# Kernel optimization log

Measured on AMD Instinct MI355X. Metric: run time of the kernel, lower is better.

Reference implementation:

```python
import jax, jax.numpy as jnp
import numpy as np

N_NODES = 100000
N_EDGES = 3200000
N_GRAPHS = 64
IN_DIM = 64
LATENT = 64
DIST_STD = 1.0


def _gcn_conv(x, W, b, src, dst, dinv):
    """PyG GCNConv: out = D^-1/2 (A+I) D^-1/2 (x W) + b, with dinv = deg^-1/2."""
    n = x.shape[0]
    h = x @ W  # [N, out]
    coef = dinv[src] * dinv[dst]  # per-edge norm
    agg = jax.ops.segment_sum(h[src] * coef[:, None], dst, num_segments=n)
    # self-loop contribution with norm dinv[i]^2
    return agg + h * (dinv * dinv)[:, None] + b


def _mean_pool(x, batch, num_graphs):
    sums = jax.ops.segment_sum(x, batch, num_segments=num_graphs)
    cnts = jax.ops.segment_sum(jnp.ones((x.shape[0],), x.dtype), batch, num_segments=num_graphs)
    return sums / jnp.maximum(cnts, 1.0)[:, None]


def setup_inputs() -> dict:
    key = jax.random.key(0)
    ks = jax.random.split(key, 12)
    x = jax.random.normal(ks[0], (N_NODES, IN_DIM), jnp.float32)
    edge_index = jax.random.randint(ks[1], (2, N_EDGES), 0, N_NODES, jnp.int64 if jax.config.jax_enable_x64 else jnp.int32).astype(jnp.int32)
    batch = jnp.sort(jax.random.randint(ks[2], (N_NODES,), 0, N_GRAPHS)).astype(jnp.int32)

    def glorot(k, shape):
        fan_in, fan_out = shape
        s = jnp.sqrt(6.0 / (fan_in + fan_out))
        return jax.random.uniform(k, shape, jnp.float32, -s, s)

    return {
        "x": x, "edge_index": edge_index, "batch": batch,
        "W1m": glorot(ks[3], (IN_DIM, 16)), "b1m": jnp.zeros((16,), jnp.float32),
        "W2m": glorot(ks[4], (16, 32)), "b2m": jnp.zeros((32,), jnp.float32),
        "W3m": glorot(ks[5], (32, LATENT)), "b3m": jnp.zeros((LATENT,), jnp.float32),
        "W1l": glorot(ks[6], (IN_DIM, 16)), "b1l": jnp.zeros((16,), jnp.float32),
        "W2l": glorot(ks[7], (16, 32)), "b2l": jnp.zeros((32,), jnp.float32),
        "W3l": glorot(ks[8], (32, LATENT)), "b3l": jnp.zeros((LATENT,), jnp.float32),
        "Wfc": glorot(ks[9], (LATENT, 160000)), "bfc": jnp.zeros((160000,), jnp.float32),
        "eps": jax.random.normal(ks[10], (N_GRAPHS, LATENT), jnp.float32) * DIST_STD,
    }


def reference(x, edge_index, batch, W1m, b1m, W2m, b2m, W3m, b3m,
              W1l, b1l, W2l, b2l, W3l, b3l, Wfc, bfc, eps):
    src, dst = edge_index[0], edge_index[1]
    n = x.shape[0]
    # degrees include self-loop (+1)
    deg = jax.ops.segment_sum(jnp.ones((src.shape[0],), x.dtype), dst, num_segments=n) + 1.0
    dinv = jax.lax.rsqrt(deg)

    mu = jax.nn.relu(_gcn_conv(x, W1m, b1m, src, dst, dinv))
    mu = jax.nn.relu(_gcn_conv(mu, W2m, b2m, src, dst, dinv))
    mu = jax.nn.relu(_gcn_conv(mu, W3m, b3m, src, dst, dinv))
    mu = _mean_pool(mu, batch, N_GRAPHS)

    log = jax.nn.relu(_gcn_conv(x, W1l, b1l, src, dst, dinv))
    log = jax.nn.relu(_gcn_conv(log, W2l, b2l, src, dst, dinv))
    log = jax.nn.relu(_gcn_conv(log, W3l, b3l, src, dst, dinv))
    logvar = _mean_pool(log, batch, N_GRAPHS)

    # latent sample (training mode): z = mu + eps * exp(0.5*logvar)
    z = mu + eps * jnp.exp(0.5 * logvar)

    # decode: sigmoid(z Wfc + bfc) -> [G, 400, 400]
    output = jax.nn.sigmoid(z @ Wfc + bfc).reshape(-1, 400, 400)
    return output, mu, logvar
```

## Files before the change

kernel.cpp:

```cpp
#include <hip/hip_runtime.h>
#include <hip/hip_bf16.h>

#define N_NODES 100000
#define N_EDGES 3200000
#define N_GRAPHS 64
#define NB 391
#define KCH 8192
#define NCHUNK ((N_EDGES + KCH - 1) / KCH)
#define MAXBKT 10240
#define NBLK3 (N_NODES / 32)

__device__ __forceinline__ void atomAddF(float* p, float v) {
    unsafeAtomicAdd(p, v);
}

__device__ __forceinline__ float lo2f(unsigned u) { return __uint_as_float(u << 16); }
__device__ __forceinline__ float hi2f(unsigned u) { return __uint_as_float(u & 0xFFFF0000u); }
__device__ __forceinline__ unsigned pack2(float a, float b) {
    unsigned ha = __bfloat16_as_ushort(__float2bfloat16(a));
    unsigned hb = __bfloat16_as_ushort(__float2bfloat16(b));
    return ha | (hb << 16);
}

__global__ __launch_bounds__(512) void k_binCount(const int* __restrict__ dst,
                                                  int* __restrict__ gcount) {
    __shared__ int hist[NB];
    for (int t = threadIdx.x; t < NB; t += 512) hist[t] = 0;
    __syncthreads();
    int base = blockIdx.x * KCH;
    int cnt = min(KCH, N_EDGES - base);
    for (int i = threadIdx.x; i < cnt; i += 512)
        atomicAdd(&hist[dst[base + i] >> 8], 1);
    __syncthreads();
    for (int t = threadIdx.x; t < NB; t += 512)
        if (hist[t]) atomicAdd(&gcount[t], hist[t]);
}

__global__ __launch_bounds__(512) void k_scanB(const int* __restrict__ gcount,
                                               int* __restrict__ gbase,
                                               int* __restrict__ gcursor,
                                               int* __restrict__ rowptr) {
    __shared__ int s[512];
    int v = (threadIdx.x < NB) ? gcount[threadIdx.x] : 0;
    s[threadIdx.x] = v;
    __syncthreads();
    for (int off = 1; off < 512; off <<= 1) {
        int t = (threadIdx.x >= off) ? s[threadIdx.x - off] : 0;
        __syncthreads();
        s[threadIdx.x] += t;
        __syncthreads();
    }
    if (threadIdx.x < NB) {
        int e = s[threadIdx.x] - v;
        gbase[threadIdx.x] = e;
        gcursor[threadIdx.x] = e;
    }
    if (threadIdx.x == 0) rowptr[N_NODES] = N_EDGES;
}

__global__ __launch_bounds__(512) void k_binA(const int* __restrict__ src,
                                              const int* __restrict__ dst,
                                              int* __restrict__ gcursor,
                                              int* __restrict__ binned) {
    __shared__ int hist[512];
    __shared__ int rbase[512];
    hist[threadIdx.x] = 0;
    __syncthreads();
    int base = blockIdx.x * KCH;
    int cnt = min(KCH, N_EDGES - base);
    int pk[16];
    int meta[16];
    #pragma unroll
    for (int i = 0; i < 16; ++i) {
        int idx = i * 512 + threadIdx.x;
        if (idx < cnt) {
            int d = dst[base + idx];
            int b = d >> 8;
            int pos = atomicAdd(&hist[b], 1);
            pk[i] = ((d & 255) << 24) | src[base + idx];
            meta[i] = (b << 13) | pos;
        } else {
            meta[i] = -1;
        }
    }
    __syncthreads();
    if (threadIdx.x < NB) {
        int v = hist[threadIdx.x];
        if (v > 0) rbase[threadIdx.x] = atomicAdd(&gcursor[threadIdx.x], v);
    }
    __syncthreads();
    #pragma unroll
    for (int i = 0; i < 16; ++i) {
        if (meta[i] >= 0) {
            int b = meta[i] >> 13;
            int pos = meta[i] & 8191;
            binned[rbase[b] + pos] = pk[i];
        }
    }
}

__global__ __launch_bounds__(512) void k_passB(const int* __restrict__ gbase,
                                               int* __restrict__ csr,
                                               int* __restrict__ rowptr,
                                               float* __restrict__ dinv) {
    int b = blockIdx.x;
    int rb = gbase[b];
    int re = (b == NB - 1) ? N_EDGES : gbase[b + 1];
    int cnt = re - rb;
    int nbase = b << 8;
    int nn = min(nbase + 256, N_NODES) - nbase;
    __shared__ int stage[MAXBKT];
    __shared__ int nhist[256];
    __shared__ int sc[256];
    __shared__ int ncur[256];
    for (int t = threadIdx.x; t < 256; t += 512) nhist[t] = 0;
    __syncthreads();
    for (int j = threadIdx.x; j < cnt; j += 512) {
        int p = csr[rb + j];
        stage[j] = p;
        atomicAdd(&nhist[((unsigned)p) >> 24], 1);
    }
    __syncthreads();
    if (threadIdx.x < 256) sc[threadIdx.x] = nhist[threadIdx.x];
    __syncthreads();
    for (int off = 1; off < 256; off <<= 1) {
        int t = (threadIdx.x < 256 && threadIdx.x >= off) ? sc[threadIdx.x - off] : 0;
        __syncthreads();
        if (threadIdx.x < 256) sc[threadIdx.x] += t;
        __syncthreads();
    }
    if (threadIdx.x < 256) {
        int e = sc[threadIdx.x] - nhist[threadIdx.x];
        ncur[threadIdx.x] = e;
        if (threadIdx.x < nn) {
            rowptr[nbase + threadIdx.x] = rb + e;
            dinv[nbase + threadIdx.x] = rsqrtf((float)nhist[threadIdx.x] + 1.0f);
        }
    }
    __syncthreads();
    for (int j = threadIdx.x; j < cnt; j += 512) {
        int p = stage[j];
        int slot = atomicAdd(&ncur[((unsigned)p) >> 24], 1);
        csr[rb + slot] = p;
    }
}

template<int LOGW, bool BIAS_RELU, bool OB, bool PRE>
__global__ void __launch_bounds__(256) k_gatherB(
        const int* __restrict__ rowptr, const int* __restrict__ csr,
        const unsigned* __restrict__ in ,
        const float* __restrict__ dinv,
        const float* __restrict__ ba, const float* __restrict__ bb,
        void* __restrict__ out) {
    constexpr int W8 = (1 << LOGW) / 8;
    constexpr int NPB = 256 / W8;
    int n = blockIdx.x * NPB + (threadIdx.x / W8);
    if (n >= N_NODES) return;
    int sub = threadIdx.x % W8;
    const uint4* in4 = (const uint4*)in;
    uint4 u = in4[(size_t)n * W8 + sub];
    float a0 = lo2f(u.x), a1 = hi2f(u.x), a2 = lo2f(u.y), a3 = hi2f(u.y);
    float a4 = lo2f(u.z), a5 = hi2f(u.z), a6 = lo2f(u.w), a7 = hi2f(u.w);
    int j = rowptr[n], end = rowptr[n + 1];
    for (; j + 8 <= end; j += 8) {
        int s0 = csr[j] & 0xFFFFFF;
        int s1 = csr[j + 1] & 0xFFFFFF;
        int s2 = csr[j + 2] & 0xFFFFFF;
        int s3 = csr[j + 3] & 0xFFFFFF;
        int s4 = csr[j + 4] & 0xFFFFFF;
        int s5 = csr[j + 5] & 0xFFFFFF;
        int s6 = csr[j + 6] & 0xFFFFFF;
        int s7 = csr[j + 7] & 0xFFFFFF;
        uint4 v0 = in4[(size_t)s0 * W8 + sub];
        uint4 v1 = in4[(size_t)s1 * W8 + sub];
        uint4 v2 = in4[(size_t)s2 * W8 + sub];
        uint4 v3 = in4[(size_t)s3 * W8 + sub];
        uint4 v4 = in4[(size_t)s4 * W8 + sub];
        uint4 v5 = in4[(size_t)s5 * W8 + sub];
        uint4 v6 = in4[(size_t)s6 * W8 + sub];
        uint4 v7 = in4[(size_t)s7 * W8 + sub];
        a0 += ((lo2f(v0.x) + lo2f(v1.x)) + (lo2f(v2.x) + lo2f(v3.x)))
            + ((lo2f(v4.x) + lo2f(v5.x)) + (lo2f(v6.x) + lo2f(v7.x)));
        a1 += ((hi2f(v0.x) + hi2f(v1.x)) + (hi2f(v2.x) + hi2f(v3.x)))
            + ((hi2f(v4.x) + hi2f(v5.x)) + (hi2f(v6.x) + hi2f(v7.x)));
        a2 += ((lo2f(v0.y) + lo2f(v1.y)) + (lo2f(v2.y) + lo2f(v3.y)))
            + ((lo2f(v4.y) + lo2f(v5.y)) + (lo2f(v6.y) + lo2f(v7.y)));
        a3 += ((hi2f(v0.y) + hi2f(v1.y)) + (hi2f(v2.y) + hi2f(v3.y)))
            + ((hi2f(v4.y) + hi2f(v5.y)) + (hi2f(v6.y) + hi2f(v7.y)));
        a4 += ((lo2f(v0.z) + lo2f(v1.z)) + (lo2f(v2.z) + lo2f(v3.z)))
            + ((lo2f(v4.z) + lo2f(v5.z)) + (lo2f(v6.z) + lo2f(v7.z)));
        a5 += ((hi2f(v0.z) + hi2f(v1.z)) + (hi2f(v2.z) + hi2f(v3.z)))
            + ((hi2f(v4.z) + hi2f(v5.z)) + (hi2f(v6.z) + hi2f(v7.z)));
        a6 += ((lo2f(v0.w) + lo2f(v1.w)) + (lo2f(v2.w) + lo2f(v3.w)))
            + ((lo2f(v4.w) + lo2f(v5.w)) + (lo2f(v6.w) + lo2f(v7.w)));
        a7 += ((hi2f(v0.w) + hi2f(v1.w)) + (hi2f(v2.w) + hi2f(v3.w)))
            + ((hi2f(v4.w) + hi2f(v5.w)) + (hi2f(v6.w) + hi2f(v7.w)));
    }
    for (; j < end; ++j) {
        int s = csr[j] & 0xFFFFFF;
        uint4 v = in4[(size_t)s * W8 + sub];
        a0 += lo2f(v.x); a1 += hi2f(v.x);
        a2 += lo2f(v.y); a3 += hi2f(v.y);
        a4 += lo2f(v.z); a5 += hi2f(v.z);
        a6 += lo2f(v.w); a7 += hi2f(v.w);
    }
    float di = dinv[n];
    a0 *= di; a1 *= di; a2 *= di; a3 *= di;
    a4 *= di; a5 *= di; a6 *= di; a7 *= di;
    if (BIAS_RELU) {
        constexpr int H = (1 << LOGW) / 2;
        int d = sub * 8;
        const float* bp = (d < H) ? (ba + d) : (bb + d - H);
        a0 = fmaxf(a0 + bp[0], 0.0f);
        a1 = fmaxf(a1 + bp[1], 0.0f);
        a2 = fmaxf(a2 + bp[2], 0.0f);
        a3 = fmaxf(a3 + bp[3], 0.0f);
        a4 = fmaxf(a4 + bp[4], 0.0f);
        a5 = fmaxf(a5 + bp[5], 0.0f);
        a6 = fmaxf(a6 + bp[6], 0.0f);
        a7 = fmaxf(a7 + bp[7], 0.0f);
    }
    if (PRE) {
        a0 *= di; a1 *= di; a2 *= di; a3 *= di;
        a4 *= di; a5 *= di; a6 *= di; a7 *= di;
    }
    if (OB) {
        ((uint4*)out)[(size_t)n * W8 + sub] =
            make_uint4(pack2(a0, a1), pack2(a2, a3), pack2(a4, a5), pack2(a6, a7));
    } else {
        constexpr int OUT4 = (1 << LOGW) / 4;
        float4* o4 = (float4*)out;
        o4[(size_t)n * OUT4 + sub * 2]     = make_float4(a0, a1, a2, a3);
        o4[(size_t)n * OUT4 + sub * 2 + 1] = make_float4(a4, a5, a6, a7);
    }
}

#define FMA4(A, W) \
    A.x = fmaf(r, W.x, A.x); A.y = fmaf(r, W.y, A.y); \
    A.z = fmaf(r, W.z, A.z); A.w = fmaf(r, W.w, A.w);

__global__ void __launch_bounds__(256) k_gd2(
        const int* __restrict__ rowptr, const int* __restrict__ csr,
        const unsigned* __restrict__ in,
        const float* __restrict__ dinv,
        const float* __restrict__ W2m, const float* __restrict__ b2m,
        const float* __restrict__ W2l, const float* __restrict__ b2l,
        unsigned* __restrict__ outB) {
    __shared__ float sW[16 * 80];
    __shared__ float agg[64 * 37];
    __shared__ float sbias[64];
    for (int t = threadIdx.x; t < 1024; t += 256) {
        int k = t >> 6, D = t & 63;
        float wv = (D < 32) ? W2m[k * 32 + D] : W2l[k * 32 + (D - 32)];
        sW[k * 80 + (D >> 4) * 20 + (D & 15)] = wv;
    }
    if (threadIdx.x < 64)
        sbias[threadIdx.x] = (threadIdx.x < 32) ? b2m[threadIdx.x]
                                                : b2l[threadIdx.x - 32];
    int ln  = threadIdx.x >> 2;
    int sub = threadIdx.x & 3;
    int n = blockIdx.x * 64 + ln;
    int nc = min(n, N_NODES - 1);
    const uint4* in4 = (const uint4*)in;
    uint4 u = in4[(size_t)nc * 4 + sub];
    float a0 = lo2f(u.x), a1 = hi2f(u.x), a2 = lo2f(u.y), a3 = hi2f(u.y);
    float a4 = lo2f(u.z), a5 = hi2f(u.z), a6 = lo2f(u.w), a7 = hi2f(u.w);
    int j = rowptr[nc], end = rowptr[nc + 1];
    for (; j + 8 <= end; j += 8) {
        int s0 = csr[j] & 0xFFFFFF;
        int s1 = csr[j + 1] & 0xFFFFFF;
        int s2 = csr[j + 2] & 0xFFFFFF;
        int s3 = csr[j + 3] & 0xFFFFFF;
        int s4 = csr[j + 4] & 0xFFFFFF;
        int s5 = csr[j + 5] & 0xFFFFFF;
        int s6 = csr[j + 6] & 0xFFFFFF;
        int s7 = csr[j + 7] & 0xFFFFFF;
        uint4 v0 = in4[(size_t)s0 * 4 + sub];
        uint4 v1 = in4[(size_t)s1 * 4 + sub];
        uint4 v2 = in4[(size_t)s2 * 4 + sub];
        uint4 v3 = in4[(size_t)s3 * 4 + sub];
        uint4 v4 = in4[(size_t)s4 * 4 + sub];
        uint4 v5 = in4[(size_t)s5 * 4 + sub];
        uint4 v6 = in4[(size_t)s6 * 4 + sub];
        uint4 v7 = in4[(size_t)s7 * 4 + sub];
        a0 += ((lo2f(v0.x) + lo2f(v1.x)) + (lo2f(v2.x) + lo2f(v3.x)))
            + ((lo2f(v4.x) + lo2f(v5.x)) + (lo2f(v6.x) + lo2f(v7.x)));
        a1 += ((hi2f(v0.x) + hi2f(v1.x)) + (hi2f(v2.x) + hi2f(v3.x)))
            + ((hi2f(v4.x) + hi2f(v5.x)) + (hi2f(v6.x) + hi2f(v7.x)));
        a2 += ((lo2f(v0.y) + lo2f(v1.y)) + (lo2f(v2.y) + lo2f(v3.y)))
            + ((lo2f(v4.y) + lo2f(v5.y)) + (lo2f(v6.y) + lo2f(v7.y)));
        a3 += ((hi2f(v0.y) + hi2f(v1.y)) + (hi2f(v2.y) + hi2f(v3.y)))
            + ((hi2f(v4.y) + hi2f(v5.y)) + (hi2f(v6.y) + hi2f(v7.y)));
        a4 += ((lo2f(v0.z) + lo2f(v1.z)) + (lo2f(v2.z) + lo2f(v3.z)))
            + ((lo2f(v4.z) + lo2f(v5.z)) + (lo2f(v6.z) + lo2f(v7.z)));
        a5 += ((hi2f(v0.z) + hi2f(v1.z)) + (hi2f(v2.z) + hi2f(v3.z)))
            + ((hi2f(v4.z) + hi2f(v5.z)) + (hi2f(v6.z) + hi2f(v7.z)));
        a6 += ((lo2f(v0.w) + lo2f(v1.w)) + (lo2f(v2.w) + lo2f(v3.w)))
            + ((lo2f(v4.w) + lo2f(v5.w)) + (lo2f(v6.w) + lo2f(v7.w)));
        a7 += ((hi2f(v0.w) + hi2f(v1.w)) + (hi2f(v2.w) + hi2f(v3.w)))
            + ((hi2f(v4.w) + hi2f(v5.w)) + (hi2f(v6.w) + hi2f(v7.w)));
    }
    for (; j < end; ++j) {
        int s = csr[j] & 0xFFFFFF;
        uint4 v = in4[(size_t)s * 4 + sub];
        a0 += lo2f(v.x); a1 += hi2f(v.x);
        a2 += lo2f(v.y); a3 += hi2f(v.y);
        a4 += lo2f(v.z); a5 += hi2f(v.z);
        a6 += lo2f(v.w); a7 += hi2f(v.w);
    }
    float di = dinv[nc];
    a0 *= di; a1 *= di; a2 *= di; a3 *= di;
    a4 *= di; a5 *= di; a6 *= di; a7 *= di;
    {
        float* ap = &agg[ln * 37 + sub * 8];
        *(float4*)&ap[0] = make_float4(a0, a1, a2, a3);
        *(float4*)&ap[4] = make_float4(a4, a5, a6, a7);
    }
    __syncthreads();

    int q = sub;
    int Dbase = q * 16;
    int koff = (q >= 2) ? 16 : 0;
    float4 c0 = *(const float4*)&sbias[Dbase];
    float4 c1 = *(const float4*)&sbias[Dbase + 4];
    float4 c2 = *(const float4*)&sbias[Dbase + 8];
    float4 c3 = *(const float4*)&sbias[Dbase + 12];
    const float* ag = &agg[ln * 37 + koff];
    const float* wq = &sW[q * 20];
    #pragma unroll
    for (int k = 0; k < 16; ++k) {
        float r = ag[k];
        const float* wr = &wq[k * 80];
        float4 w0 = *(const float4*)&wr[0];
        float4 w1 = *(const float4*)&wr[4];
        float4 w2 = *(const float4*)&wr[8];
        float4 w3 = *(const float4*)&wr[12];
        FMA4(c0, w0)
        FMA4(c1, w1)
        FMA4(c2, w2)
        FMA4(c3, w3)
    }
    c0.x = fmaxf(c0.x, 0.f) * di; c0.y = fmaxf(c0.y, 0.f) * di;
    c0.z = fmaxf(c0.z, 0.f) * di; c0.w = fmaxf(c0.w, 0.f) * di;
    c1.x = fmaxf(c1.x, 0.f) * di; c1.y = fmaxf(c1.y, 0.f) * di;
    c1.z = fmaxf(c1.z, 0.f) * di; c1.w = fmaxf(c1.w, 0.f) * di;
    c2.x = fmaxf(c2.x, 0.f) * di; c2.y = fmaxf(c2.y, 0.f) * di;
    c2.z = fmaxf(c2.z, 0.f) * di; c2.w = fmaxf(c2.w, 0.f) * di;
    c3.x = fmaxf(c3.x, 0.f) * di; c3.y = fmaxf(c3.y, 0.f) * di;
    c3.z = fmaxf(c3.z, 0.f) * di; c3.w = fmaxf(c3.w, 0.f) * di;
    if (n < N_NODES) {
        uint4* o4 = (uint4*)outB;
        o4[(size_t)n * 8 + q * 2] =
            make_uint4(pack2(c0.x, c0.y), pack2(c0.z, c0.w),
                       pack2(c1.x, c1.y), pack2(c1.z, c1.w));
        o4[(size_t)n * 8 + q * 2 + 1] =
            make_uint4(pack2(c2.x, c2.y), pack2(c2.z, c2.w),
                       pack2(c3.x, c3.y), pack2(c3.z, c3.w));
    }
}

__global__ void __launch_bounds__(256) k_gd3(
        const int* __restrict__ rowptr, const int* __restrict__ csr,
        const unsigned* __restrict__ in,
        const float* __restrict__ dinv,
        const float* __restrict__ W3m, const float* __restrict__ b3m,
        const float* __restrict__ W3l, const float* __restrict__ b3l,
        const int* __restrict__ batch,
        float* __restrict__ part0, float* __restrict__ part1,
        int* __restrict__ pg0, int* __restrict__ pg1) {
    __shared__ float s_ali[32 * 160];
    __shared__ float agg[32 * 68];
    __shared__ float sbias[128];
    __shared__ int   sbatch[32];
    __shared__ int   ssplit;
    float* sWall = s_ali;
    float* h3s   = s_ali;

    for (int t = threadIdx.x; t < 4096; t += 256) {
        int k = t >> 7, D = t & 127;
        float wv = (D < 64) ? W3m[k * 64 + D] : W3l[k * 64 + (D - 64)];
        sWall[k * 160 + (D >> 4) * 20 + (D & 15)] = wv;
    }
    if (threadIdx.x < 128)
        sbias[threadIdx.x] = (threadIdx.x < 64) ? b3m[threadIdx.x]
                                                : b3l[threadIdx.x - 64];
    int nbase = blockIdx.x * 32;
    if (threadIdx.x < 32) sbatch[threadIdx.x] = batch[nbase + threadIdx.x];

    int ln  = threadIdx.x >> 3;
    int sub = threadIdx.x & 7;
    int n = nbase + ln;
    const uint4* in4 = (const uint4*)in;
    uint4 u = in4[(size_t)n * 8 + sub];
    float a0 = lo2f(u.x), a1 = hi2f(u.x), a2 = lo2f(u.y), a3 = hi2f(u.y);
    float a4 = lo2f(u.z), a5 = hi2f(u.z), a6 = lo2f(u.w), a7 = hi2f(u.w);
    int j = rowptr[n], end = rowptr[n + 1];
    for (; j + 8 <= end; j += 8) {
        int s0 = csr[j] & 0xFFFFFF;
        int s1 = csr[j + 1] & 0xFFFFFF;
        int s2 = csr[j + 2] & 0xFFFFFF;
        int s3 = csr[j + 3] & 0xFFFFFF;
        int s4 = csr[j + 4] & 0xFFFFFF;
        int s5 = csr[j + 5] & 0xFFFFFF;
        int s6 = csr[j + 6] & 0xFFFFFF;
        int s7 = csr[j + 7] & 0xFFFFFF;
        uint4 v0 = in4[(size_t)s0 * 8 + sub];
        uint4 v1 = in4[(size_t)s1 * 8 + sub];
        uint4 v2 = in4[(size_t)s2 * 8 + sub];
        uint4 v3 = in4[(size_t)s3 * 8 + sub];
        uint4 v4 = in4[(size_t)s4 * 8 + sub];
        uint4 v5 = in4[(size_t)s5 * 8 + sub];
        uint4 v6 = in4[(size_t)s6 * 8 + sub];
        uint4 v7 = in4[(size_t)s7 * 8 + sub];
        a0 += ((lo2f(v0.x) + lo2f(v1.x)) + (lo2f(v2.x) + lo2f(v3.x)))
            + ((lo2f(v4.x) + lo2f(v5.x)) + (lo2f(v6.x) + lo2f(v7.x)));
        a1 += ((hi2f(v0.x) + hi2f(v1.x)) + (hi2f(v2.x) + hi2f(v3.x)))
            + ((hi2f(v4.x) + hi2f(v5.x)) + (hi2f(v6.x) + hi2f(v7.x)));
        a2 += ((lo2f(v0.y) + lo2f(v1.y)) + (lo2f(v2.y) + lo2f(v3.y)))
            + ((lo2f(v4.y) + lo2f(v5.y)) + (lo2f(v6.y) + lo2f(v7.y)));
        a3 += ((hi2f(v0.y) + hi2f(v1.y)) + (hi2f(v2.y) + hi2f(v3.y)))
            + ((hi2f(v4.y) + hi2f(v5.y)) + (hi2f(v6.y) + hi2f(v7.y)));
        a4 += ((lo2f(v0.z) + lo2f(v1.z)) + (lo2f(v2.z) + lo2f(v3.z)))
            + ((lo2f(v4.z) + lo2f(v5.z)) + (lo2f(v6.z) + lo2f(v7.z)));
        a5 += ((hi2f(v0.z) + hi2f(v1.z)) + (hi2f(v2.z) + hi2f(v3.z)))
            + ((hi2f(v4.z) + hi2f(v5.z)) + (hi2f(v6.z) + hi2f(v7.z)));
        a6 += ((lo2f(v0.w) + lo2f(v1.w)) + (lo2f(v2.w) + lo2f(v3.w)))
            + ((lo2f(v4.w) + lo2f(v5.w)) + (lo2f(v6.w) + lo2f(v7.w)));
        a7 += ((hi2f(v0.w) + hi2f(v1.w)) + (hi2f(v2.w) + hi2f(v3.w)))
            + ((hi2f(v4.w) + hi2f(v5.w)) + (hi2f(v6.w) + hi2f(v7.w)));
    }
    for (; j < end; ++j) {
        int s = csr[j] & 0xFFFFFF;
        uint4 v = in4[(size_t)s * 8 + sub];
        a0 += lo2f(v.x); a1 += hi2f(v.x);
        a2 += lo2f(v.y); a3 += hi2f(v.y);
        a4 += lo2f(v.z); a5 += hi2f(v.z);
        a6 += lo2f(v.w); a7 += hi2f(v.w);
    }
    float di = dinv[n];
    a0 *= di; a1 *= di; a2 *= di; a3 *= di;
    a4 *= di; a5 *= di; a6 *= di; a7 *= di;
    {
        float* ap = &agg[ln * 68 + sub * 8];
        *(float4*)&ap[0] = make_float4(a0, a1, a2, a3);
        *(float4*)&ap[4] = make_float4(a4, a5, a6, a7);
    }
    if (threadIdx.x == 0) {
        int sp = 32;
        int ga = sbatch[0];
        for (int i = 1; i < 32; ++i)
            if (sbatch[i] != ga) { sp = i; break; }
        ssplit = sp;
    }
    __syncthreads();

    int ln2 = threadIdx.x >> 3;
    int q   = threadIdx.x & 7;
    int Dbase = q * 16;
    int koff = (q >= 4) ? 32 : 0;
    float4 c0 = *(const float4*)&sbias[Dbase];
    float4 c1 = *(const float4*)&sbias[Dbase + 4];
    float4 c2 = *(const float4*)&sbias[Dbase + 8];
    float4 c3 = *(const float4*)&sbias[Dbase + 12];
    const float* ag = &agg[ln2 * 68 + koff];
    const float* wq = &sWall[q * 20];
    #pragma unroll
    for (int k = 0; k < 32; ++k) {
        float r = ag[k];
        const float* wr = &wq[k * 160];
        float4 w0 = *(const float4*)&wr[0];
        float4 w1 = *(const float4*)&wr[4];
        float4 w2 = *(const float4*)&wr[8];
        float4 w3 = *(const float4*)&wr[12];
        FMA4(c0, w0)
        FMA4(c1, w1)
        FMA4(c2, w2)
        FMA4(c3, w3)
    }
    c0.x = fmaxf(c0.x, 0.f); c0.y = fmaxf(c0.y, 0.f);
    c0.z = fmaxf(c0.z, 0.f); c0.w = fmaxf(c0.w, 0.f);
    c1.x = fmaxf(c1.x, 0.f); c1.y = fmaxf(c1.y, 0.f);
    c1.z = fmaxf(c1.z, 0.f); c1.w = fmaxf(c1.w, 0.f);
    c2.x = fmaxf(c2.x, 0.f); c2.y = fmaxf(c2.y, 0.f);
    c2.z = fmaxf(c2.z, 0.f); c2.w = fmaxf(c2.w, 0.f);
    c3.x = fmaxf(c3.x, 0.f); c3.y = fmaxf(c3.y, 0.f);
    c3.z = fmaxf(c3.z, 0.f); c3.w = fmaxf(c3.w, 0.f);
    __syncthreads();

    {
        float* hp = &h3s[ln2 * 132 + Dbase];
        *(float4*)&hp[0]  = c0;
        *(float4*)&hp[4]  = c1;
        *(float4*)&hp[8]  = c2;
        *(float4*)&hp[12] = c3;
    }
    __syncthreads();
    {
        int d    = threadIdx.x & 127;
        int slot = threadIdx.x >> 7;
        int sp = ssplit;
        int s = slot ? sp : 0;
        int e = slot ? 32 : sp;
        float acc = 0.f;
        for (int nn = s; nn < e; ++nn)
            acc += h3s[nn * 132 + d];
        int blk = blockIdx.x;
        if (slot == 0) {
            part0[(size_t)blk * 128 + d] = acc;
            if (d == 0) pg0[blk] = sbatch[0];
        } else {
            part1[(size_t)blk * 128 + d] = acc;
            if (d == 0) pg1[blk] = (sp < 32) ? sbatch[31] : -1;
        }
    }
}

__global__ void __launch_bounds__(128) k_poolF(
        const float* __restrict__ part0, const float* __restrict__ part1,
        const int* __restrict__ pg0, const int* __restrict__ pg1,
        const int* __restrict__ batch, const float* __restrict__ eps,
        float* __restrict__ zbuf, float* __restrict__ out_mu,
        float* __restrict__ out_lv) {
    int g = blockIdx.x;
    __shared__ int sb[2];
    __shared__ float spool[128];
    if (threadIdx.x < 2) {
        int target = g + threadIdx.x;
        int lo = 0, hi = N_NODES;
        while (lo < hi) {
            int mid = (lo + hi) >> 1;
            if (batch[mid] < target) lo = mid + 1; else hi = mid;
        }
        sb[threadIdx.x] = lo;
    }
    __syncthreads();
    int ns = sb[0], ne = sb[1];
    int d = threadIdx.x;
    float acc = 0.f;
    if (ne > ns) {
        int b0 = ns >> 5, b1 = (ne - 1) >> 5;
        for (int b = b0; b <= b1; ++b) {
            if (pg0[b] == g) acc += part0[(size_t)b * 128 + d];
            if (pg1[b] == g) acc += part1[(size_t)b * 128 + d];
        }
    }
    spool[d] = acc;
    __syncthreads();
    if (threadIdx.x < 64) {
        int k = threadIdx.x;
        float c = fmaxf((float)(ne - ns), 1.0f);
        float mu = spool[k] / c;
        float lv = spool[64 + k] / c;
        zbuf[k * 64 + g] = mu + eps[g * 64 + k] * __expf(0.5f * lv);
        out_mu[g * 64 + k] = mu;
        out_lv[g * 64 + k] = lv;
    }
}

template<int IN_W, int OUT_HALF, int A_OFF, int A_W, int B_OFF, bool BR, bool OB, bool DS>
__global__ void k_dense4(const float* __restrict__ in,
                         const float* __restrict__ Wa, const float* __restrict__ ba,
                         const float* __restrict__ Wb, const float* __restrict__ bb,
                         const float* __restrict__ dinv,
                         void* __restrict__ out) {
    __shared__ float sWa[A_W * OUT_HALF];
    __shared__ float sWb[A_W * OUT_HALF];
    __shared__ float sba[OUT_HALF];
    __shared__ float sbb[OUT_HALF];
    for (int t = threadIdx.x; t < A_W * OUT_HALF; t += 256) {
        sWa[t] = Wa[t];
        sWb[t] = Wb[t];
    }
    if (BR && threadIdx.x < OUT_HALF) {
        sba[threadIdx.x] = ba[threadIdx.x];
        sbb[threadIdx.x] = bb[threadIdx.x];
    }
    __syncthreads();
    constexpr int TPN = OUT_HALF / 2;
    int idx = blockIdx.x * 256 + threadIdx.x;
    int n = idx / TPN;
    int q = idx % TPN;
    bool isB = (q * 4) >= OUT_HALF;
    int dd = q * 4 - (isB ? OUT_HALF : 0);
    const float* sW = isB ? sWb : sWa;
    int ko = isB ? B_OFF : A_OFF;
    float4 acc;
    if (BR) {
        const float* bp = isB ? (sbb + dd) : (sba + dd);
        acc = make_float4(bp[0], bp[1], bp[2], bp[3]);
    } else {
        acc = make_float4(0.f, 0.f, 0.f, 0.f);
    }
    const float* row = in + (size_t)n * IN_W + ko;
    #pragma unroll
    for (int k = 0; k < A_W; ++k) {
        float r = row[k];
        float4 wv = *(const float4*)&sW[k * OUT_HALF + dd];
        acc.x = fmaf(r, wv.x, acc.x);
        acc.y = fmaf(r, wv.y, acc.y);
        acc.z = fmaf(r, wv.z, acc.z);
        acc.w = fmaf(r, wv.w, acc.w);
    }
    if (BR) {
        acc.x = fmaxf(acc.x, 0.f); acc.y = fmaxf(acc.y, 0.f);
        acc.z = fmaxf(acc.z, 0.f); acc.w = fmaxf(acc.w, 0.f);
    }
    if (DS) {
        float dn = dinv[n];
        acc.x *= dn; acc.y *= dn; acc.z *= dn; acc.w *= dn;
    }
    if (OB) {
        ((uint2*)out)[idx] = make_uint2(pack2(acc.x, acc.y), pack2(acc.z, acc.w));
    } else {
        ((float4*)out)[idx] = acc;
    }
}

__global__ void __launch_bounds__(256) k_decode(const float* __restrict__ zT,
                                                const float* __restrict__ Wfc,
                                                const float* __restrict__ bfc,
                                                float* __restrict__ out) {
    int j = (blockIdx.x >> 1) * 256 + threadIdx.x;
    int gh = (blockIdx.x & 1) * 32;
    const float* zp = zT + gh;
    float bias = bfc[j];
    float acc[32];
    #pragma unroll
    for (int g = 0; g < 32; ++g) acc[g] = bias;
    #pragma unroll 8
    for (int k = 0; k < 64; ++k) {
        float w = Wfc[(size_t)k * 160000 + j];
        #pragma unroll
        for (int g = 0; g < 32; ++g)
            acc[g] = fmaf(zp[k * 64 + g], w, acc[g]);
    }
    #pragma unroll
    for (int g = 0; g < 32; ++g) {
        float s = 1.0f / (1.0f + __expf(-acc[g]));
        out[(size_t)(gh + g) * 160000 + j] = s;
    }
}

extern "C" void kernel_launch(void* const* d_in, const int* in_sizes, int n_in,
                              void* d_out, int out_size, void* d_ws, size_t ws_size,
                              hipStream_t stream) {
    const float* x     = (const float*)d_in[0];
    const int*   ei    = (const int*)d_in[1];
    const int*   batch = (const int*)d_in[2];
    const float *W1m = (const float*)d_in[3],  *b1m = (const float*)d_in[4];
    const float *W2m = (const float*)d_in[5],  *b2m = (const float*)d_in[6];
    const float *W3m = (const float*)d_in[7],  *b3m = (const float*)d_in[8];
    const float *W1l = (const float*)d_in[9],  *b1l = (const float*)d_in[10];
    const float *W2l = (const float*)d_in[11], *b2l = (const float*)d_in[12];
    const float *W3l = (const float*)d_in[13], *b3l = (const float*)d_in[14];
    const float *Wfc = (const float*)d_in[15], *bfc = (const float*)d_in[16];
    const float *eps = (const float*)d_in[17];

    const int* srcv = ei;
    const int* dstv = ei + N_EDGES;

    char* w = (char*)d_ws;
    auto alloc = [&](size_t bytes) -> char* {
        char* p = w;
        w += (bytes + 255) & ~(size_t)255;
        return p;
    };
    int*   gcount = (int*)  alloc((size_t)NB * 4);
    int*   gbase  = (int*)  alloc((size_t)NB * 4);
    int*   gcursor= (int*)  alloc((size_t)NB * 4);
    int*   rowptr = (int*)  alloc((size_t)(N_NODES + 1) * 4);
    float* dinv   = (float*)alloc((size_t)N_NODES * 4);
    float* zbuf   = (float*)alloc((size_t)N_GRAPHS * 64 * 4);
    float* arena = (float*)alloc((size_t)N_NODES * 192 * 4);
    float* A   = arena;
    float* B   = arena + (size_t)N_NODES * 64;
    int*   csr = (int*)(arena + (size_t)N_NODES * 128);
    float* B2  = arena + (size_t)N_NODES * 160;
    float* part0 = A;
    float* part1 = A + (size_t)NBLK3 * 128;
    int*   pg0   = (int*)(A + (size_t)2 * NBLK3 * 128);
    int*   pg1   = pg0 + NBLK3;

    float* out    = (float*)d_out;
    float* out_mu = out + 10240000;
    float* out_lv = out + 10240000 + 4096;

    hipMemsetAsync(gcount, 0, (size_t)NB * 4, stream);

    k_binCount<<<NCHUNK, 512, 0, stream>>>(dstv, gcount);
    k_scanB<<<1, 512, 0, stream>>>(gcount, gbase, gcursor, rowptr);
    k_binA<<<NCHUNK, 512, 0, stream>>>(srcv, dstv, gcursor, csr);
    k_passB<<<NB, 512, 0, stream>>>(gbase, csr, rowptr, dinv);

    k_dense4<64, 16, 0, 64, 0, false, true, true><<<N_NODES * 8 / 256, 256, 0, stream>>>(
        x, W1m, b1m, W1l, b1l, dinv, A);
    k_gatherB<5, true, true, true><<<(N_NODES + 63) / 64, 256, 0, stream>>>(
        rowptr, csr, (const unsigned*)A, dinv, b1m, b1l, B);

    k_gd2<<<(N_NODES + 63) / 64, 256, 0, stream>>>(
        rowptr, csr, (const unsigned*)B, dinv, W2m, b2m, W2l, b2l, (unsigned*)B2);

    k_gd3<<<NBLK3, 256, 0, stream>>>(
        rowptr, csr, (const unsigned*)B2, dinv, W3m, b3m, W3l, b3l, batch,
        part0, part1, pg0, pg1);

    k_poolF<<<N_GRAPHS, 128, 0, stream>>>(part0, part1, pg0, pg1, batch, eps,
                                          zbuf, out_mu, out_lv);

    k_decode<<<1250, 256, 0, stream>>>(zbuf, Wfc, bfc, out);
}
```

Before: 434.6 us.

## Drop edge-count pass via fixed-capacity buckets; widen gd3 blocks to 64 nodes

Removes the separate bin-counting kernel and its read of dst. Edges are now scattered directly into fixed-capacity per-bucket regions of size MAXBKT, with offsets computed by a scan of the final cursors. This saves one full pass over the destination indices and a launch, but relies on no bucket exceeding MAXBKT entries, which the random input makes likely rather than guaranteed. The final gather-dense-pool kernel is also reorganised to 64 nodes per 512-thread block, with bounds clamping and matching pooling indices.

```diff
diff --git a/kernel.cpp b/kernel.cpp
--- a/kernel.cpp
+++ b/kernel.cpp
@@ -8,7 +8,7 @@
 #define KCH 8192
 #define NCHUNK ((N_EDGES + KCH - 1) / KCH)
 #define MAXBKT 10240
-#define NBLK3 (N_NODES / 32)
+#define NBLK3B 1563
 
 __device__ __forceinline__ void atomAddF(float* p, float v) {
     unsafeAtomicAdd(p, v);
@@ -22,46 +22,10 @@
     return ha | (hb << 16);
 }
 
-__global__ __launch_bounds__(512) void k_binCount(const int* __restrict__ dst,
-                                                  int* __restrict__ gcount) {
-    __shared__ int hist[NB];
-    for (int t = threadIdx.x; t < NB; t += 512) hist[t] = 0;
-    __syncthreads();
-    int base = blockIdx.x * KCH;
-    int cnt = min(KCH, N_EDGES - base);
-    for (int i = threadIdx.x; i < cnt; i += 512)
-        atomicAdd(&hist[dst[base + i] >> 8], 1);
-    __syncthreads();
-    for (int t = threadIdx.x; t < NB; t += 512)
-        if (hist[t]) atomicAdd(&gcount[t], hist[t]);
-}
-
-__global__ __launch_bounds__(512) void k_scanB(const int* __restrict__ gcount,
-                                               int* __restrict__ gbase,
-                                               int* __restrict__ gcursor,
-                                               int* __restrict__ rowptr) {
-    __shared__ int s[512];
-    int v = (threadIdx.x < NB) ? gcount[threadIdx.x] : 0;
-    s[threadIdx.x] = v;
-    __syncthreads();
-    for (int off = 1; off < 512; off <<= 1) {
-        int t = (threadIdx.x >= off) ? s[threadIdx.x - off] : 0;
-        __syncthreads();
-        s[threadIdx.x] += t;
-        __syncthreads();
-    }
-    if (threadIdx.x < NB) {
-        int e = s[threadIdx.x] - v;
-        gbase[threadIdx.x] = e;
-        gcursor[threadIdx.x] = e;
-    }
-    if (threadIdx.x == 0) rowptr[N_NODES] = N_EDGES;
-}
-
 __global__ __launch_bounds__(512) void k_binA(const int* __restrict__ src,
                                               const int* __restrict__ dst,
                                               int* __restrict__ gcursor,
-                                              int* __restrict__ binned) {
+                                              int* __restrict__ bins) {
     __shared__ int hist[512];
     __shared__ int rbase[512];
     hist[threadIdx.x] = 0;
@@ -94,12 +58,30 @@
         if (meta[i] >= 0) {
             int b = meta[i] >> 13;
             int pos = meta[i] & 8191;
-            binned[rbase[b] + pos] = pk[i];
+            bins[(size_t)b * MAXBKT + rbase[b] + pos] = pk[i];
         }
     }
 }
 
+__global__ __launch_bounds__(512) void k_scanB2(const int* __restrict__ gcursor,
+                                                int* __restrict__ gbase,
+                                                int* __restrict__ rowptr) {
+    __shared__ int s[512];
+    int v = (threadIdx.x < NB) ? gcursor[threadIdx.x] : 0;
+    s[threadIdx.x] = v;
+    __syncthreads();
+    for (int off = 1; off < 512; off <<= 1) {
+        int t = (threadIdx.x >= off) ? s[threadIdx.x - off] : 0;
+        __syncthreads();
+        s[threadIdx.x] += t;
+        __syncthreads();
+    }
+    if (threadIdx.x < NB) gbase[threadIdx.x] = s[threadIdx.x] - v;
+    if (threadIdx.x == 0) rowptr[N_NODES] = N_EDGES;
+}
+
 __global__ __launch_bounds__(512) void k_passB(const int* __restrict__ gbase,
+                                               const int* __restrict__ bins,
                                                int* __restrict__ csr,
                                                int* __restrict__ rowptr,
                                                float* __restrict__ dinv) {
@@ -115,8 +97,9 @@
     __shared__ int ncur[256];
     for (int t = threadIdx.x; t < 256; t += 512) nhist[t] = 0;
     __syncthreads();
+    const int* bsrc = bins + (size_t)b * MAXBKT;
     for (int j = threadIdx.x; j < cnt; j += 512) {
-        int p = csr[rb + j];
+        int p = bsrc[j];
         stage[j] = p;
         atomicAdd(&nhist[((unsigned)p) >> 24], 1);
     }
@@ -359,7 +342,8 @@
     }
 }
 
-__global__ void __launch_bounds__(256) k_gd3(
+__global__ void __launch_bounds__(512) void_marker();
+__global__ void __launch_bounds__(512) k_gd3(
         const int* __restrict__ rowptr, const int* __restrict__ csr,
         const unsigned* __restrict__ in,
         const float* __restrict__ dinv,
@@ -368,15 +352,15 @@
         const int* __restrict__ batch,
         float* __restrict__ part0, float* __restrict__ part1,
         int* __restrict__ pg0, int* __restrict__ pg1) {
-    __shared__ float s_ali[32 * 160];
-    __shared__ float agg[32 * 68];
+    __shared__ float s_ali[64 * 132];
+    __shared__ float agg[64 * 68];
     __shared__ float sbias[128];
-    __shared__ int   sbatch[32];
+    __shared__ int   sbatch[64];
     __shared__ int   ssplit;
     float* sWall = s_ali;
     float* h3s   = s_ali;
 
-    for (int t = threadIdx.x; t < 4096; t += 256) {
+    for (int t = threadIdx.x; t < 4096; t += 512) {
         int k = t >> 7, D = t & 127;
         float wv = (D < 64) ? W3m[k * 64 + D] : W3l[k * 64 + (D - 64)];
         sWall[k * 160 + (D >> 4) * 20 + (D & 15)] = wv;
@@ -384,17 +368,19 @@
     if (threadIdx.x < 128)
         sbias[threadIdx.x] = (threadIdx.x < 64) ? b3m[threadIdx.x]
                                                 : b3l[threadIdx.x - 64];
-    int nbase = blockIdx.x * 32;
-    if (threadIdx.x < 32) sbatch[threadIdx.x] = batch[nbase + threadIdx.x];
+    int nbase = blockIdx.x * 64;
+    if (threadIdx.x < 64)
+        sbatch[threadIdx.x] = batch[min(nbase + (int)threadIdx.x, N_NODES - 1)];
 
     int ln  = threadIdx.x >> 3;
     int sub = threadIdx.x & 7;
     int n = nbase + ln;
+    int nc = min(n, N_NODES - 1);
     const uint4* in4 = (const uint4*)in;
-    uint4 u = in4[(size_t)n * 8 + sub];
+    uint4 u = in4[(size_t)nc * 8 + sub];
     float a0 = lo2f(u.x), a1 = hi2f(u.x), a2 = lo2f(u.y), a3 = hi2f(u.y);
     float a4 = lo2f(u.z), a5 = hi2f(u.z), a6 = lo2f(u.w), a7 = hi2f(u.w);
-    int j = rowptr[n], end = rowptr[n + 1];
+    int j = rowptr[nc], end = rowptr[nc + 1];
     for (; j + 8 <= end; j += 8) {
         int s0 = csr[j] & 0xFFFFFF;
         int s1 = csr[j + 1] & 0xFFFFFF;
@@ -437,7 +423,7 @@
         a4 += lo2f(v.z); a5 += hi2f(v.z);
         a6 += lo2f(v.w); a7 += hi2f(v.w);
     }
-    float di = dinv[n];
+    float di = dinv[nc];
     a0 *= di; a1 *= di; a2 *= di; a3 *= di;
     a4 *= di; a5 *= di; a6 *= di; a7 *= di;
     {
@@ -446,9 +432,9 @@
         *(float4*)&ap[4] = make_float4(a4, a5, a6, a7);
     }
     if (threadIdx.x == 0) {
-        int sp = 32;
+        int sp = 64;
         int ga = sbatch[0];
-        for (int i = 1; i < 32; ++i)
+        for (int i = 1; i < 64; ++i)
             if (sbatch[i] != ga) { sp = i; break; }
         ssplit = sp;
     }
@@ -495,12 +481,13 @@
         *(float4*)&hp[12] = c3;
     }
     __syncthreads();
-    {
+    if (threadIdx.x < 256) {
         int d    = threadIdx.x & 127;
         int slot = threadIdx.x >> 7;
-        int sp = ssplit;
+        int ncap = min(64, N_NODES - nbase);
+        int sp = min(ssplit, ncap);
         int s = slot ? sp : 0;
-        int e = slot ? 32 : sp;
+        int e = slot ? ncap : sp;
         float acc = 0.f;
         for (int nn = s; nn < e; ++nn)
             acc += h3s[nn * 132 + d];
@@ -510,7 +497,7 @@
             if (d == 0) pg0[blk] = sbatch[0];
         } else {
             part1[(size_t)blk * 128 + d] = acc;
-            if (d == 0) pg1[blk] = (sp < 32) ? sbatch[31] : -1;
+            if (d == 0) pg1[blk] = (sp < ncap) ? sbatch[63] : -1;
         }
     }
 }
@@ -538,7 +525,7 @@
     int d = threadIdx.x;
     float acc = 0.f;
     if (ne > ns) {
-        int b0 = ns >> 5, b1 = (ne - 1) >> 5;
+        int b0 = ns >> 6, b1 = (ne - 1) >> 6;
         for (int b = b0; b <= b1; ++b) {
             if (pg0[b] == g) acc += part0[(size_t)b * 128 + d];
             if (pg1[b] == g) acc += part1[(size_t)b * 128 + d];
@@ -665,7 +652,6 @@
         w += (bytes + 255) & ~(size_t)255;
         return p;
     };
-    int*   gcount = (int*)  alloc((size_t)NB * 4);
     int*   gbase  = (int*)  alloc((size_t)NB * 4);
     int*   gcursor= (int*)  alloc((size_t)NB * 4);
     int*   rowptr = (int*)  alloc((size_t)(N_NODES + 1) * 4);
@@ -676,21 +662,21 @@
     float* B   = arena + (size_t)N_NODES * 64;
     int*   csr = (int*)(arena + (size_t)N_NODES * 128);
     float* B2  = arena + (size_t)N_NODES * 160;
+    int*   bins  = (int*)A;
     float* part0 = A;
-    float* part1 = A + (size_t)NBLK3 * 128;
-    int*   pg0   = (int*)(A + (size_t)2 * NBLK3 * 128);
-    int*   pg1   = pg0 + NBLK3;
+    float* part1 = A + (size_t)NBLK3B * 128;
+    int*   pg0   = (int*)(A + (size_t)2 * NBLK3B * 128);
+    int*   pg1   = pg0 + NBLK3B;
 
     float* out    = (float*)d_out;
     float* out_mu = out + 10240000;
     float* out_lv = out + 10240000 + 4096;
 
-    hipMemsetAsync(gcount, 0, (size_t)NB * 4, stream);
-
-    k_binCount<<<NCHUNK, 512, 0, stream>>>(dstv, gcount);
-    k_scanB<<<1, 512, 0, stream>>>(gcount, gbase, gcursor, rowptr);
-    k_binA<<<NCHUNK, 512, 0, stream>>>(srcv, dstv, gcursor, csr);
-    k_passB<<<NB, 512, 0, stream>>>(gbase, csr, rowptr, dinv);
+    hipMemsetAsync(gcursor, 0, (size_t)NB * 4, stream);
+
+    k_binA<<<NCHUNK, 512, 0, stream>>>(srcv, dstv, gcursor, bins);
+    k_scanB2<<<1, 512, 0, stream>>>(gcursor, gbase, rowptr);
+    k_passB<<<NB, 512, 0, stream>>>(gbase, bins, csr, rowptr, dinv);
 
     k_dense4<64, 16, 0, 64, 0, false, true, true><<<N_NODES * 8 / 256, 256, 0, stream>>>(
         x, W1m, b1m, W1l, b1l, dinv, A);
@@ -700,7 +686,7 @@
     k_gd2<<<(N_NODES + 63) / 64, 256, 0, stream>>>(
         rowptr, csr, (const unsigned*)B, dinv, W2m, b2m, W2l, b2l, (unsigned*)B2);
 
-    k_gd3<<<NBLK3, 256, 0, stream>>>(
+    k_gd3<<<NBLK3B, 512, 0, stream>>>(
         rowptr, csr, (const unsigned*)B2, dinv, W3m, b3m, W3l, b3l, batch,
         part0, part1, pg0, pg1);
 
```

After: 432.8 us. About the same (-0.4%).

## Bin edges into fixed-capacity buckets to drop the separate counting pass

Applied to the files above, without the earlier changes.

Edges are now scattered straight into per-bucket slots of fixed capacity MAXBKT, using a zeroed cursor, so the separate dst histogram pass over all edges is no longer needed. A small scan over the final bucket cursors then gives the bucket bases, and the CSR build reads each bucket from its fixed slot. This saves one full read of the dst array and one kernel launch. The cost is a larger scratch region laid over A, and correctness assumes no bucket holds more than MAXBKT edges.

```diff
diff --git a/kernel.cpp b/kernel.cpp
--- a/kernel.cpp
+++ b/kernel.cpp
@@ -22,46 +22,10 @@
     return ha | (hb << 16);
 }
 
-__global__ __launch_bounds__(512) void k_binCount(const int* __restrict__ dst,
-                                                  int* __restrict__ gcount) {
-    __shared__ int hist[NB];
-    for (int t = threadIdx.x; t < NB; t += 512) hist[t] = 0;
-    __syncthreads();
-    int base = blockIdx.x * KCH;
-    int cnt = min(KCH, N_EDGES - base);
-    for (int i = threadIdx.x; i < cnt; i += 512)
-        atomicAdd(&hist[dst[base + i] >> 8], 1);
-    __syncthreads();
-    for (int t = threadIdx.x; t < NB; t += 512)
-        if (hist[t]) atomicAdd(&gcount[t], hist[t]);
-}
-
-__global__ __launch_bounds__(512) void k_scanB(const int* __restrict__ gcount,
-                                               int* __restrict__ gbase,
-                                               int* __restrict__ gcursor,
-                                               int* __restrict__ rowptr) {
-    __shared__ int s[512];
-    int v = (threadIdx.x < NB) ? gcount[threadIdx.x] : 0;
-    s[threadIdx.x] = v;
-    __syncthreads();
-    for (int off = 1; off < 512; off <<= 1) {
-        int t = (threadIdx.x >= off) ? s[threadIdx.x - off] : 0;
-        __syncthreads();
-        s[threadIdx.x] += t;
-        __syncthreads();
-    }
-    if (threadIdx.x < NB) {
-        int e = s[threadIdx.x] - v;
-        gbase[threadIdx.x] = e;
-        gcursor[threadIdx.x] = e;
-    }
-    if (threadIdx.x == 0) rowptr[N_NODES] = N_EDGES;
-}
-
 __global__ __launch_bounds__(512) void k_binA(const int* __restrict__ src,
                                               const int* __restrict__ dst,
                                               int* __restrict__ gcursor,
-                                              int* __restrict__ binned) {
+                                              int* __restrict__ bins) {
     __shared__ int hist[512];
     __shared__ int rbase[512];
     hist[threadIdx.x] = 0;
@@ -94,12 +58,30 @@
         if (meta[i] >= 0) {
             int b = meta[i] >> 13;
             int pos = meta[i] & 8191;
-            binned[rbase[b] + pos] = pk[i];
+            bins[(size_t)b * MAXBKT + rbase[b] + pos] = pk[i];
         }
     }
 }
 
+__global__ __launch_bounds__(512) void k_scanB2(const int* __restrict__ gcursor,
+                                                int* __restrict__ gbase,
+                                                int* __restrict__ rowptr) {
+    __shared__ int s[512];
+    int v = (threadIdx.x < NB) ? gcursor[threadIdx.x] : 0;
+    s[threadIdx.x] = v;
+    __syncthreads();
+    for (int off = 1; off < 512; off <<= 1) {
+        int t = (threadIdx.x >= off) ? s[threadIdx.x - off] : 0;
+        __syncthreads();
+        s[threadIdx.x] += t;
+        __syncthreads();
+    }
+    if (threadIdx.x < NB) gbase[threadIdx.x] = s[threadIdx.x] - v;
+    if (threadIdx.x == 0) rowptr[N_NODES] = N_EDGES;
+}
+
 __global__ __launch_bounds__(512) void k_passB(const int* __restrict__ gbase,
+                                               const int* __restrict__ bins,
                                                int* __restrict__ csr,
                                                int* __restrict__ rowptr,
                                                float* __restrict__ dinv) {
@@ -115,8 +97,9 @@
     __shared__ int ncur[256];
     for (int t = threadIdx.x; t < 256; t += 512) nhist[t] = 0;
     __syncthreads();
+    const int* bsrc = bins + (size_t)b * MAXBKT;
     for (int j = threadIdx.x; j < cnt; j += 512) {
-        int p = csr[rb + j];
+        int p = bsrc[j];
         stage[j] = p;
         atomicAdd(&nhist[((unsigned)p) >> 24], 1);
     }
@@ -665,7 +648,6 @@
         w += (bytes + 255) & ~(size_t)255;
         return p;
     };
-    int*   gcount = (int*)  alloc((size_t)NB * 4);
     int*   gbase  = (int*)  alloc((size_t)NB * 4);
     int*   gcursor= (int*)  alloc((size_t)NB * 4);
     int*   rowptr = (int*)  alloc((size_t)(N_NODES + 1) * 4);
@@ -676,6 +658,7 @@
     float* B   = arena + (size_t)N_NODES * 64;
     int*   csr = (int*)(arena + (size_t)N_NODES * 128);
     float* B2  = arena + (size_t)N_NODES * 160;
+    int*   bins  = (int*)A;
     float* part0 = A;
     float* part1 = A + (size_t)NBLK3 * 128;
     int*   pg0   = (int*)(A + (size_t)2 * NBLK3 * 128);
@@ -685,12 +668,11 @@
     float* out_mu = out + 10240000;
     float* out_lv = out + 10240000 + 4096;
 
-    hipMemsetAsync(gcount, 0, (size_t)NB * 4, stream);
-
-    k_binCount<<<NCHUNK, 512, 0, stream>>>(dstv, gcount);
-    k_scanB<<<1, 512, 0, stream>>>(gcount, gbase, gcursor, rowptr);
-    k_binA<<<NCHUNK, 512, 0, stream>>>(srcv, dstv, gcursor, csr);
-    k_passB<<<NB, 512, 0, stream>>>(gbase, csr, rowptr, dinv);
+    hipMemsetAsync(gcursor, 0, (size_t)NB * 4, stream);
+
+    k_binA<<<NCHUNK, 512, 0, stream>>>(srcv, dstv, gcursor, bins);
+    k_scanB2<<<1, 512, 0, stream>>>(gcursor, gbase, rowptr);
+    k_passB<<<NB, 512, 0, stream>>>(gbase, bins, csr, rowptr, dinv);
 
     k_dense4<64, 16, 0, 64, 0, false, true, true><<<N_NODES * 8 / 256, 256, 0, stream>>>(
         x, W1m, b1m, W1l, b1l, dinv, A);
```

Result: faster. 424.7 us (-2.3%).
